# Kernel tuning notes

Measured on AMD Instinct MI355X. Metric: run time of the kernel, lower is better.

Reference implementation:

```python
import jax, jax.numpy as jnp
import numpy as np

B, S, D, H = 2, 2048, 1024, 16
HD = D // H
NEG = -9e15


def setup_inputs() -> dict:
    key = jax.random.key(0)
    ks = jax.random.split(key, 4)
    x = jax.random.normal(ks[0], (B, S, D), dtype=jnp.float32)
    # causal mask, broadcastable over batch and heads
    mask = jnp.tril(jnp.ones((S, S), dtype=jnp.int32))[None, None]
    W_qkv = jax.random.normal(ks[1], (D, 3 * D), dtype=jnp.float32) * (1.0 / np.sqrt(D))
    b_qkv = jnp.zeros((3 * D,), dtype=jnp.float32)
    W_out = jax.random.normal(ks[2], (D, D), dtype=jnp.float32) * (1.0 / np.sqrt(D))
    b_out = jnp.zeros((D,), dtype=jnp.float32)
    return {"x": x, "mask": mask, "W_qkv": W_qkv, "b_qkv": b_qkv,
            "W_out": W_out, "b_out": b_out}


def reference(x, mask, W_qkv, b_qkv, W_out, b_out):
    b, s, _ = x.shape
    qkv = x @ W_qkv + b_qkv                       # [B,S,3D]
    qkv = qkv.reshape(b, s, H, 3 * HD)            # per-head interleaved qkv
    qkv = jnp.transpose(qkv, (0, 2, 1, 3))        # [B,H,S,3*HD]
    q, k, v = jnp.split(qkv, 3, axis=-1)          # each [B,H,S,HD]
    scores = jnp.einsum('bhqd,bhkd->bhqk', q, k) / np.sqrt(HD)
    scores = jnp.where(mask == 0, jnp.float32(NEG), scores)
    attn = jax.nn.softmax(scores, axis=-1)
    out = jnp.einsum('bhqk,bhkd->bhqd', attn, v)  # [B,H,S,HD]
    out = jnp.transpose(out, (0, 2, 1, 3)).reshape(b, s, H * HD)
    return out @ W_out + b_out
```

## Files before the change

### kernel.cpp

```cpp
#include <hip/hip_runtime.h>
#include <math.h>

constexpr int Bb = 2, Ss = 2048, Dd = 1024, Hh = 16, HDd = 64;

typedef __attribute__((ext_vector_type(8))) short bf16x8;
typedef __attribute__((ext_vector_type(4))) float f32x4;
typedef __attribute__((ext_vector_type(8))) unsigned short u16x8;
typedef __attribute__((ext_vector_type(4))) unsigned short u16x4;

__device__ __forceinline__ unsigned short bf16_rn(float f) {
  unsigned int u = __float_as_uint(f);
  u += 0x7fffu + ((u >> 16) & 1u);
  return (unsigned short)(u >> 16);
}
__device__ __forceinline__ float bf16_f(unsigned short h) {
  return __uint_as_float(((unsigned int)h) << 16);
}

__global__ __launch_bounds__(256) void split_f32(
    const float* __restrict__ in, unsigned short* __restrict__ hi,
    unsigned short* __restrict__ lo, int n8) {
  int i = blockIdx.x * 256 + threadIdx.x;
  if (i >= n8) return;
  const float4* p = (const float4*)in + (size_t)i * 2;
  float4 a = p[0], b = p[1];
  float v[8] = {a.x, a.y, a.z, a.w, b.x, b.y, b.z, b.w};
  u16x8 h, l;
  #pragma unroll
  for (int j = 0; j < 8; j++) {
    unsigned short hb = bf16_rn(v[j]);
    h[j] = hb;
    l[j] = bf16_rn(v[j] - bf16_f(hb));
  }
  *(u16x8*)(hi + (size_t)i * 8) = h;
  *(u16x8*)(lo + (size_t)i * 8) = l;
}

__global__ __launch_bounds__(256) void transpose_split_f32(
    const float* __restrict__ W, unsigned short* __restrict__ Thi,
    unsigned short* __restrict__ Tlo, int K, int N) {
  __shared__ float tile[32][33];
  int n0 = blockIdx.x * 32, k0 = blockIdx.y * 32;
  int t = threadIdx.x;
  #pragma unroll
  for (int p = 0; p < 4; p++) {
    int idx = t + p * 256;
    int kk = idx >> 5, nn = idx & 31;
    tile[kk][nn] = W[(size_t)(k0 + kk) * N + n0 + nn];
  }
  __syncthreads();
  #pragma unroll
  for (int p = 0; p < 4; p++) {
    int idx = t + p * 256;
    int nn = idx >> 5, kk = idx & 31;
    float v = tile[kk][nn];
    unsigned short hb = bf16_rn(v);
    size_t o = (size_t)(n0 + nn) * K + k0 + kk;
    Thi[o] = hb;
    Tlo[o] = bf16_rn(v - bf16_f(hb));
  }
}

typedef __attribute__((address_space(3))) unsigned int lds_u32;
typedef const __attribute__((address_space(1))) unsigned int glb_u32;
__device__ __forceinline__ void gload16(const void* g, void* l) {
  __builtin_amdgcn_global_load_lds((glb_u32*)g, (lds_u32*)l, 16, 0, 0);
}

#define GEMM_CORE(KD)                                                          \
  __shared__ unsigned short lds[4 * 4096];                                     \
  const int tid = threadIdx.x;                                                 \
  const int lane = tid & 63, wid = tid >> 6;                                   \
  const int m0 = blockIdx.y * 128, n0 = blockIdx.x * 128;                      \
  const int wrow = wid >> 1, wcol = wid & 1;                                   \
  const int lrow = lane & 15, g = lane >> 4;                                   \
  const int o0 = wid * 128 + lane, o1 = o0 + 64;                               \
  const int r0 = o0 >> 2, G0 = (o0 & 3) ^ ((r0 >> 1) & 3);                     \
  const int r1 = o1 >> 2, G1 = (o1 & 3) ^ ((r1 >> 1) & 3);                     \
  const unsigned short* sA0h = Ahi + (size_t)(m0 + r0) * KD + G0 * 8;          \
  const unsigned short* sA1h = Ahi + (size_t)(m0 + r1) * KD + G1 * 8;          \
  const unsigned short* sA0l = Alo + (size_t)(m0 + r0) * KD + G0 * 8;          \
  const unsigned short* sA1l = Alo + (size_t)(m0 + r1) * KD + G1 * 8;          \
  const unsigned short* sB0h = Bhi + (size_t)(n0 + r0) * KD + G0 * 8;          \
  const unsigned short* sB1h = Bhi + (size_t)(n0 + r1) * KD + G1 * 8;          \
  const unsigned short* sB0l = Blo + (size_t)(n0 + r0) * KD + G0 * 8;          \
  const unsigned short* sB1l = Blo + (size_t)(n0 + r1) * KD + G1 * 8;          \
  unsigned short* dA0h = lds + 0 + wid * 1024;                                 \
  unsigned short* dA1h = dA0h + 512;                                           \
  unsigned short* dA0l = lds + 4096 + wid * 1024;                              \
  unsigned short* dA1l = dA0l + 512;                                           \
  unsigned short* dB0h = lds + 8192 + wid * 1024;                              \
  unsigned short* dB1h = dB0h + 512;                                           \
  unsigned short* dB0l = lds + 12288 + wid * 1024;                             \
  unsigned short* dB1l = dB0l + 512;                                           \
  int offA[4], offB[4];                                                        \
  _Pragma("unroll")                                                            \
  for (int m = 0; m < 4; m++) {                                                \
    int row = wrow * 64 + m * 16 + lrow;                                       \
    offA[m] = row * 32 + ((g ^ ((row >> 1) & 3)) * 8);                         \
  }                                                                            \
  _Pragma("unroll")                                                            \
  for (int n = 0; n < 4; n++) {                                                \
    int row = wcol * 64 + n * 16 + lrow;                                       \
    offB[n] = row * 32 + ((g ^ ((row >> 1) & 3)) * 8);                         \
  }                                                                            \
  f32x4 acc[4][4];                                                             \
  _Pragma("unroll")                                                            \
  for (int m = 0; m < 4; m++)                                                  \
    _Pragma("unroll")                                                          \
    for (int n = 0; n < 4; n++) acc[m][n] = (f32x4){0.f, 0.f, 0.f, 0.f};       \
  for (int k0 = 0; k0 < KD; k0 += 32) {                                        \
    gload16(sA0h + k0, dA0h); gload16(sA1h + k0, dA1h);                        \
    gload16(sA0l + k0, dA0l); gload16(sA1l + k0, dA1l);                        \
    gload16(sB0h + k0, dB0h); gload16(sB1h + k0, dB1h);                        \
    gload16(sB0l + k0, dB0l); gload16(sB1l + k0, dB1l);                        \
    __syncthreads();                                                           \
    bf16x8 ah[4], al[4], bh[4], bl[4];                                         \
    _Pragma("unroll")                                                          \
    for (int m = 0; m < 4; m++) {                                              \
      ah[m] = *(const bf16x8*)(lds + 0 + offA[m]);                             \
      al[m] = *(const bf16x8*)(lds + 4096 + offA[m]);                          \
    }                                                                          \
    _Pragma("unroll")                                                          \
    for (int n = 0; n < 4; n++) {                                              \
      bh[n] = *(const bf16x8*)(lds + 8192 + offB[n]);                          \
      bl[n] = *(const bf16x8*)(lds + 12288 + offB[n]);                         \
    }                                                                          \
    _Pragma("unroll")                                                          \
    for (int m = 0; m < 4; m++)                                                \
      _Pragma("unroll")                                                        \
      for (int n = 0; n < 4; n++) {                                            \
        acc[m][n] = __builtin_amdgcn_mfma_f32_16x16x32_bf16(ah[m], bh[n], acc[m][n], 0, 0, 0); \
        acc[m][n] = __builtin_amdgcn_mfma_f32_16x16x32_bf16(ah[m], bl[n], acc[m][n], 0, 0, 0); \
        acc[m][n] = __builtin_amdgcn_mfma_f32_16x16x32_bf16(al[m], bh[n], acc[m][n], 0, 0, 0); \
      }                                                                        \
    __syncthreads();                                                           \
  }

template<int KD>
__global__ __launch_bounds__(256) void gemm_split_bf16(
    const unsigned short* __restrict__ Ahi, const unsigned short* __restrict__ Alo,
    const unsigned short* __restrict__ Bhi, const unsigned short* __restrict__ Blo,
    const float* __restrict__ bias, float* __restrict__ C, int N)
{
  GEMM_CORE(KD)
  #pragma unroll
  for (int n = 0; n < 4; n++) {
    int gcol = n0 + wcol * 64 + n * 16 + lrow;
    float bv = bias[gcol];
    #pragma unroll
    for (int m = 0; m < 4; m++) {
      f32x4 a = acc[m][n];
      #pragma unroll
      for (int r = 0; r < 4; r++) {
        int grow = m0 + wrow * 64 + m * 16 + g * 4 + r;
        C[(size_t)grow * N + gcol] = a[r] + bv;
      }
    }
  }
}

template<int KD>
__global__ __launch_bounds__(256) void gemm_qkv(
    const unsigned short* __restrict__ Ahi, const unsigned short* __restrict__ Alo,
    const unsigned short* __restrict__ Bhi, const unsigned short* __restrict__ Blo,
    const float* __restrict__ bias,
    unsigned short* __restrict__ Qh, unsigned short* __restrict__ Ql,
    unsigned short* __restrict__ Kh, unsigned short* __restrict__ Kl,
    unsigned short* __restrict__ Vth, unsigned short* __restrict__ Vtl)
{
  GEMM_CORE(KD)
  const int bidx = m0 >> 11;
  const int sbase = (m0 & 2047) + wrow * 64 + g * 4;
  #pragma unroll
  for (int n = 0; n < 4; n++) {
    int gcol = n0 + wcol * 64 + n * 16 + lrow;
    unsigned hh = (unsigned)gcol / 192u;
    int inner = gcol - (int)hh * 192;
    int part = inner >> 6;
    int d = inner & 63;
    float bv = bias[gcol];
    size_t base = (size_t)(bidx * 16 + (int)hh) * 131072;
    #pragma unroll
    for (int m = 0; m < 4; m++) {
      f32x4 a = acc[m][n];
      int s0 = sbase + m * 16;
      if (part == 0) {
        #pragma unroll
        for (int r = 0; r < 4; r++) {
          float v = (a[r] + bv) * 0.18033688011112042f;
          unsigned short hi = bf16_rn(v);
          size_t ix = base + (size_t)(s0 + r) * 64 + d;
          Qh[ix] = hi; Ql[ix] = bf16_rn(v - bf16_f(hi));
        }
      } else if (part == 1) {
        #pragma unroll
        for (int r = 0; r < 4; r++) {
          float v = a[r] + bv;
          unsigned short hi = bf16_rn(v);
          size_t ix = base + (size_t)(s0 + r) * 64 + d;
          Kh[ix] = hi; Kl[ix] = bf16_rn(v - bf16_f(hi));
        }
      } else {
        u16x4 hv, lv;
        #pragma unroll
        for (int r = 0; r < 4; r++) {
          float v = a[r] + bv;
          hv[r] = bf16_rn(v);
          lv[r] = bf16_rn(v - bf16_f(hv[r]));
        }
        size_t ix = base + (size_t)d * 2048 + s0;
        *(u16x4*)(Vth + ix) = hv;
        *(u16x4*)(Vtl + ix) = lv;
      }
    }
  }
}

__global__ __launch_bounds__(512) void flash_attn_mfma(
    const unsigned short* __restrict__ Qh, const unsigned short* __restrict__ Ql,
    const unsigned short* __restrict__ Kh, const unsigned short* __restrict__ Kl,
    const unsigned short* __restrict__ Vth, const unsigned short* __restrict__ Vtl,
    unsigned short* __restrict__ atthi, unsigned short* __restrict__ attlo)
{
  const int pidx = blockIdx.x;
  const int h = blockIdx.y, b = blockIdx.z;
  const int bh = b * Hh + h;
  const int NT = Ss / 128;
  const int qtA = pidx, qtB = NT - 1 - pidx;
  const int tid = threadIdx.x, lane = tid & 63, wid = tid >> 6;
  const int q0w = (wid < 4) ? (qtA * 128 + wid * 32)
                            : (qtB * 128 + (wid - 4) * 32);
  const int lrow = lane & 15, lg = lane >> 4;

  __shared__ unsigned short KH[2][4096], KL[2][4096], VH[2][4096], VL[2][4096];
  __shared__ unsigned short Pbuf[8][2048];

  const size_t hb = (size_t)bh * 131072;
  const unsigned short* qhb = Qh + hb;
  const unsigned short* qlb = Ql + hb;
  const unsigned short* khb = Kh + hb;
  const unsigned short* klb = Kl + hb;
  const unsigned short* vhb = Vth + hb;
  const unsigned short* vlb = Vtl + hb;

  bf16x8 qfh[2][2], qfl[2][2];
  #pragma unroll
  for (int mi = 0; mi < 2; mi++)
    #pragma unroll
    for (int ks = 0; ks < 2; ks++) {
      int off = (q0w + mi * 16 + lrow) * 64 + ks * 32 + lg * 8;
      qfh[mi][ks] = *(const bf16x8*)(qhb + off);
      qfl[mi][ks] = *(const bf16x8*)(qlb + off);
    }

  int offK[4][2], offP[2][2];
  #pragma unroll
  for (int ci = 0; ci < 4; ci++)
    #pragma unroll
    for (int ks = 0; ks < 2; ks++) {
      int row = ci * 16 + lrow;
      offK[ci][ks] = row * 64 + (((ks * 4 + lg) ^ (row & 7)) * 8);
    }
  #pragma unroll
  for (int mi = 0; mi < 2; mi++)
    #pragma unroll
    for (int ks = 0; ks < 2; ks++) {
      int row = mi * 16 + lrow;
      offP[mi][ks] = row * 64 + (((ks * 4 + lg) ^ (row & 7)) * 8);
    }

  const int sr = tid >> 3, sg = ((tid & 7) ^ ((tid >> 3) & 7)) * 8;

  float m_[2][4], l_[2][4];
  f32x4 oacc[2][4];
  #pragma unroll
  for (int mi = 0; mi < 2; mi++)
    #pragma unroll
    for (int r = 0; r < 4; r++) { m_[mi][r] = -INFINITY; l_[mi][r] = 0.f; }
  #pragma unroll
  for (int mi = 0; mi < 2; mi++)
    #pragma unroll
    for (int di = 0; di < 4; di++) oacc[mi][di] = (f32x4){0.f, 0.f, 0.f, 0.f};

  unsigned short* Pw = Pbuf[wid];
  const int nt = 2 * (qtB + 1);

  gload16(khb + (size_t)sr * 64 + sg, KH[0] + wid * 512);
  gload16(klb + (size_t)sr * 64 + sg, KL[0] + wid * 512);
  gload16(vhb + (size_t)sr * 2048 + sg, VH[0] + wid * 512);
  gload16(vlb + (size_t)sr * 2048 + sg, VL[0] + wid * 512);
  __syncthreads();

  for (int t = 0; t < nt; ++t) {
    const int kv0 = t * 64;
    if (t + 1 < nt) {
      const int nb = (t + 1) & 1;
      const int nk = kv0 + 64;
      gload16(khb + (size_t)(nk + sr) * 64 + sg, KH[nb] + wid * 512);
      gload16(klb + (size_t)(nk + sr) * 64 + sg, KL[nb] + wid * 512);
      gload16(vhb + (size_t)sr * 2048 + nk + sg, VH[nb] + wid * 512);
      gload16(vlb + (size_t)sr * 2048 + nk + sg, VL[nb] + wid * 512);
    }

    if (kv0 <= q0w + 31) {
      const int cb = t & 1;
      const unsigned short* KHc = KH[cb];
      const unsigned short* KLc = KL[cb];
      const unsigned short* VHc = VH[cb];
      const unsigned short* VLc = VL[cb];

      f32x4 sf[2][4];
      #pragma unroll
      for (int mi = 0; mi < 2; mi++)
        #pragma unroll
        for (int ci = 0; ci < 4; ci++) sf[mi][ci] = (f32x4){0.f, 0.f, 0.f, 0.f};
      __builtin_amdgcn_s_setprio(1);
      #pragma unroll
      for (int ci = 0; ci < 4; ci++) {
        bf16x8 kh0 = *(const bf16x8*)(KHc + offK[ci][0]);
        bf16x8 kh1 = *(const bf16x8*)(KHc + offK[ci][1]);
        bf16x8 kl0 = *(const bf16x8*)(KLc + offK[ci][0]);
        bf16x8 kl1 = *(const bf16x8*)(KLc + offK[ci][1]);
        #pragma unroll
        for (int mi = 0; mi < 2; mi++) {
          f32x4 s = sf[mi][ci];
          s = __builtin_amdgcn_mfma_f32_16x16x32_bf16(qfh[mi][0], kh0, s, 0, 0, 0);
          s = __builtin_amdgcn_mfma_f32_16x16x32_bf16(qfh[mi][1], kh1, s, 0, 0, 0);
          s = __builtin_amdgcn_mfma_f32_16x16x32_bf16(qfh[mi][0], kl0, s, 0, 0, 0);
          s = __builtin_amdgcn_mfma_f32_16x16x32_bf16(qfh[mi][1], kl1, s, 0, 0, 0);
          s = __builtin_amdgcn_mfma_f32_16x16x32_bf16(qfl[mi][0], kh0, s, 0, 0, 0);
          s = __builtin_amdgcn_mfma_f32_16x16x32_bf16(qfl[mi][1], kh1, s, 0, 0, 0);
          sf[mi][ci] = s;
        }
      }
      __builtin_amdgcn_s_setprio(0);

      if (kv0 + 63 > q0w) {
        #pragma unroll
        for (int mi = 0; mi < 2; mi++)
          #pragma unroll
          for (int ci = 0; ci < 4; ci++)
            #pragma unroll
            for (int r = 0; r < 4; r++) {
              int q = q0w + mi * 16 + lg * 4 + r;
              int kv = kv0 + ci * 16 + lrow;
              if (kv > q) sf[mi][ci][r] = -1e30f;
            }
      }

      #pragma unroll
      for (int mi = 0; mi < 2; mi++)
        #pragma unroll
        for (int r = 0; r < 4; r++) {
          float mx = fmaxf(fmaxf(sf[mi][0][r], sf[mi][1][r]),
                           fmaxf(sf[mi][2][r], sf[mi][3][r]));
          mx = fmaxf(mx, __shfl_xor(mx, 1));
          mx = fmaxf(mx, __shfl_xor(mx, 2));
          mx = fmaxf(mx, __shfl_xor(mx, 4));
          mx = fmaxf(mx, __shfl_xor(mx, 8));
          float mn = fmaxf(m_[mi][r], mx);
          float alpha = __builtin_amdgcn_exp2f(m_[mi][r] - mn);
          m_[mi][r] = mn;
          float rs = 0.f;
          #pragma unroll
          for (int ci = 0; ci < 4; ci++) {
            float p = __builtin_amdgcn_exp2f(sf[mi][ci][r] - mn);
            sf[mi][ci][r] = p;
            rs += p;
          }
          rs += __shfl_xor(rs, 1);
          rs += __shfl_xor(rs, 2);
          rs += __shfl_xor(rs, 4);
          rs += __shfl_xor(rs, 8);
          l_[mi][r] = l_[mi][r] * alpha + rs;
          #pragma unroll
          for (int di = 0; di < 4; di++) oacc[mi][di][r] *= alpha;
        }

      #pragma unroll
      for (int mi = 0; mi < 2; mi++)
        #pragma unroll
        for (int ci = 0; ci < 4; ci++) {
          int colb = ci * 16 + lrow;
          int gcol = colb >> 3, crem = colb & 7;
          #pragma unroll
          for (int r = 0; r < 4; r++) {
            int rr = mi * 16 + lg * 4 + r;
            Pw[rr * 64 + ((gcol ^ (rr & 7)) * 8) + crem] = bf16_rn(sf[mi][ci][r]);
          }
        }

      bf16x8 pa[2][2];
      #pragma unroll
      for (int mi = 0; mi < 2; mi++)
        #pragma unroll
        for (int ks = 0; ks < 2; ks++)
          pa[mi][ks] = *(const bf16x8*)(Pw + offP[mi][ks]);
      __builtin_amdgcn_s_setprio(1);
      #pragma unroll
      for (int di = 0; di < 4; di++) {
        bf16x8 vh0 = *(const bf16x8*)(VHc + offK[di][0]);
        bf16x8 vh1 = *(const bf16x8*)(VHc + offK[di][1]);
        bf16x8 vl0 = *(const bf16x8*)(VLc + offK[di][0]);
        bf16x8 vl1 = *(const bf16x8*)(VLc + offK[di][1]);
        #pragma unroll
        for (int mi = 0; mi < 2; mi++) {
          f32x4 o = oacc[mi][di];
          o = __builtin_amdgcn_mfma_f32_16x16x32_bf16(pa[mi][0], vh0, o, 0, 0, 0);
          o = __builtin_amdgcn_mfma_f32_16x16x32_bf16(pa[mi][1], vh1, o, 0, 0, 0);
          o = __builtin_amdgcn_mfma_f32_16x16x32_bf16(pa[mi][0], vl0, o, 0, 0, 0);
          o = __builtin_amdgcn_mfma_f32_16x16x32_bf16(pa[mi][1], vl1, o, 0, 0, 0);
          oacc[mi][di] = o;
        }
      }
      __builtin_amdgcn_s_setprio(0);
    }
    __syncthreads();
  }

  #pragma unroll
  for (int mi = 0; mi < 2; mi++) {
    float inv[4];
    #pragma unroll
    for (int r = 0; r < 4; r++) inv[r] = 1.f / l_[mi][r];
    #pragma unroll
    for (int di = 0; di < 4; di++) {
      f32x4 o = oacc[mi][di];
      #pragma unroll
      for (int r = 0; r < 4; r++) {
        float v = o[r] * inv[r];
        int srow = q0w + mi * 16 + lg * 4 + r;
        size_t idx = ((size_t)b * Ss + srow) * 1024 + h * 64 + di * 16 + lrow;
        unsigned short hi = bf16_rn(v);
        atthi[idx] = hi;
        attlo[idx] = bf16_rn(v - bf16_f(hi));
      }
    }
  }
}

extern "C" void kernel_launch(void* const* d_in, const int* in_sizes, int n_in,
                              void* d_out, int out_size, void* d_ws, size_t ws_size,
                              hipStream_t stream) {
  const float* x    = (const float*)d_in[0];
  const float* Wqkv = (const float*)d_in[2];
  const float* bqkv = (const float*)d_in[3];
  const float* Wout = (const float*)d_in[4];
  const float* bout = (const float*)d_in[5];
  float* out = (float*)d_out;

  char* ws = (char*)d_ws;
  unsigned short* Qh  = (unsigned short*)(ws);
  unsigned short* Ql  = (unsigned short*)(ws + 8388608);
  unsigned short* Kh  = (unsigned short*)(ws + 16777216);
  unsigned short* Kl  = (unsigned short*)(ws + 25165824);
  unsigned short* Vth = (unsigned short*)(ws + 33554432);
  unsigned short* Vtl = (unsigned short*)(ws + 41943040);
  unsigned short* atthi = (unsigned short*)(ws + 50331648);
  unsigned short* attlo = (unsigned short*)(ws + 58720256);
  unsigned short* xhi = (unsigned short*)(ws + 67108864);
  unsigned short* xlo = (unsigned short*)(ws + 75497472);
  unsigned short* wqh = (unsigned short*)(ws + 83886080);
  unsigned short* wql = (unsigned short*)(ws + 90177536);
  unsigned short* woh = (unsigned short*)(ws + 96468992);
  unsigned short* wol = (unsigned short*)(ws + 98566144);

  const int M = Bb * Ss;

  split_f32<<<(M * Dd / 8) / 256, 256, 0, stream>>>(x, xhi, xlo, M * Dd / 8);
  transpose_split_f32<<<dim3(3 * Dd / 32, Dd / 32), 256, 0, stream>>>(Wqkv, wqh, wql, Dd, 3 * Dd);
  transpose_split_f32<<<dim3(Dd / 32, Dd / 32), 256, 0, stream>>>(Wout, woh, wol, Dd, Dd);

  gemm_qkv<1024><<<dim3(3 * Dd / 128, M / 128), 256, 0, stream>>>(
      xhi, xlo, wqh, wql, bqkv, Qh, Ql, Kh, Kl, Vth, Vtl);

  flash_attn_mfma<<<dim3(Ss / 256, Hh, Bb), 512, 0, stream>>>(
      Qh, Ql, Kh, Kl, Vth, Vtl, atthi, attlo);

  gemm_split_bf16<1024><<<dim3(Dd / 128, M / 128), 256, 0, stream>>>(
      atthi, attlo, woh, wol, bout, out, Dd);
}
```

Before: 355.5 us.

## Double-buffer split-bf16 GEMMs with 512-thread blocks and larger QKV tiles

Replaces the single-buffered GEMM macro with a templated core that prefetches the next K-slice into a second LDS buffer using global_load_lds, with explicit vmcnt waits and raw barriers. It uses 8 waves per block, a 256x192 tile for the QKV projection and a 128x128 tile with 8 waves for the output projection, and raises MFMA wave priority with s_setprio. The aim is to overlap global loads with MFMA work and to raise data reuse per block. In exchange it uses more LDS and registers (24 accumulators per wave in QKV), and the QKV grid shrinks to 256 blocks, which may leave the CU array partly idle.

```diff
diff --git a/kernel.cpp b/kernel.cpp
--- a/kernel.cpp
+++ b/kernel.cpp
@@ -67,101 +67,154 @@
   __builtin_amdgcn_global_load_lds((glb_u32*)g, (lds_u32*)l, 16, 0, 0);
 }
 
-#define GEMM_CORE(KD)                                                          \
-  __shared__ unsigned short lds[4 * 4096];                                     \
-  const int tid = threadIdx.x;                                                 \
-  const int lane = tid & 63, wid = tid >> 6;                                   \
-  const int m0 = blockIdx.y * 128, n0 = blockIdx.x * 128;                      \
-  const int wrow = wid >> 1, wcol = wid & 1;                                   \
-  const int lrow = lane & 15, g = lane >> 4;                                   \
-  const int o0 = wid * 128 + lane, o1 = o0 + 64;                               \
-  const int r0 = o0 >> 2, G0 = (o0 & 3) ^ ((r0 >> 1) & 3);                     \
-  const int r1 = o1 >> 2, G1 = (o1 & 3) ^ ((r1 >> 1) & 3);                     \
-  const unsigned short* sA0h = Ahi + (size_t)(m0 + r0) * KD + G0 * 8;          \
-  const unsigned short* sA1h = Ahi + (size_t)(m0 + r1) * KD + G1 * 8;          \
-  const unsigned short* sA0l = Alo + (size_t)(m0 + r0) * KD + G0 * 8;          \
-  const unsigned short* sA1l = Alo + (size_t)(m0 + r1) * KD + G1 * 8;          \
-  const unsigned short* sB0h = Bhi + (size_t)(n0 + r0) * KD + G0 * 8;          \
-  const unsigned short* sB1h = Bhi + (size_t)(n0 + r1) * KD + G1 * 8;          \
-  const unsigned short* sB0l = Blo + (size_t)(n0 + r0) * KD + G0 * 8;          \
-  const unsigned short* sB1l = Blo + (size_t)(n0 + r1) * KD + G1 * 8;          \
-  unsigned short* dA0h = lds + 0 + wid * 1024;                                 \
-  unsigned short* dA1h = dA0h + 512;                                           \
-  unsigned short* dA0l = lds + 4096 + wid * 1024;                              \
-  unsigned short* dA1l = dA0l + 512;                                           \
-  unsigned short* dB0h = lds + 8192 + wid * 1024;                              \
-  unsigned short* dB1h = dB0h + 512;                                           \
-  unsigned short* dB0l = lds + 12288 + wid * 1024;                             \
-  unsigned short* dB1l = dB0l + 512;                                           \
-  int offA[4], offB[4];                                                        \
-  _Pragma("unroll")                                                            \
-  for (int m = 0; m < 4; m++) {                                                \
-    int row = wrow * 64 + m * 16 + lrow;                                       \
-    offA[m] = row * 32 + ((g ^ ((row >> 1) & 3)) * 8);                         \
-  }                                                                            \
-  _Pragma("unroll")                                                            \
-  for (int n = 0; n < 4; n++) {                                                \
-    int row = wcol * 64 + n * 16 + lrow;                                       \
-    offB[n] = row * 32 + ((g ^ ((row >> 1) & 3)) * 8);                         \
-  }                                                                            \
-  f32x4 acc[4][4];                                                             \
-  _Pragma("unroll")                                                            \
-  for (int m = 0; m < 4; m++)                                                  \
-    _Pragma("unroll")                                                          \
-    for (int n = 0; n < 4; n++) acc[m][n] = (f32x4){0.f, 0.f, 0.f, 0.f};       \
-  for (int k0 = 0; k0 < KD; k0 += 32) {                                        \
-    gload16(sA0h + k0, dA0h); gload16(sA1h + k0, dA1h);                        \
-    gload16(sA0l + k0, dA0l); gload16(sA1l + k0, dA1l);                        \
-    gload16(sB0h + k0, dB0h); gload16(sB1h + k0, dB1h);                        \
-    gload16(sB0l + k0, dB0l); gload16(sB1l + k0, dB1l);                        \
-    __syncthreads();                                                           \
-    bf16x8 ah[4], al[4], bh[4], bl[4];                                         \
-    _Pragma("unroll")                                                          \
-    for (int m = 0; m < 4; m++) {                                              \
-      ah[m] = *(const bf16x8*)(lds + 0 + offA[m]);                             \
-      al[m] = *(const bf16x8*)(lds + 4096 + offA[m]);                          \
-    }                                                                          \
-    _Pragma("unroll")                                                          \
-    for (int n = 0; n < 4; n++) {                                              \
-      bh[n] = *(const bf16x8*)(lds + 8192 + offB[n]);                          \
-      bl[n] = *(const bf16x8*)(lds + 12288 + offB[n]);                         \
-    }                                                                          \
-    _Pragma("unroll")                                                          \
-    for (int m = 0; m < 4; m++)                                                \
-      _Pragma("unroll")                                                        \
-      for (int n = 0; n < 4; n++) {                                            \
-        acc[m][n] = __builtin_amdgcn_mfma_f32_16x16x32_bf16(ah[m], bh[n], acc[m][n], 0, 0, 0); \
-        acc[m][n] = __builtin_amdgcn_mfma_f32_16x16x32_bf16(ah[m], bl[n], acc[m][n], 0, 0, 0); \
-        acc[m][n] = __builtin_amdgcn_mfma_f32_16x16x32_bf16(al[m], bh[n], acc[m][n], 0, 0, 0); \
-      }                                                                        \
-    __syncthreads();                                                           \
-  }
-
-template<int KD>
-__global__ __launch_bounds__(256) void gemm_split_bf16(
+__device__ __forceinline__ void syncb() {
+  asm volatile("" ::: "memory");
+  __builtin_amdgcn_s_barrier();
+  asm volatile("" ::: "memory");
+}
+template<int N> __device__ __forceinline__ void wait_vmcnt() {
+  if constexpr (N == 0)      asm volatile("s_waitcnt vmcnt(0)" ::: "memory");
+  else if constexpr (N == 4) asm volatile("s_waitcnt vmcnt(4)" ::: "memory");
+  else if constexpr (N == 7) asm volatile("s_waitcnt vmcnt(7)" ::: "memory");
+}
+
+template<int BM, int BN>
+__device__ __forceinline__ void gemm_core256(
     const unsigned short* __restrict__ Ahi, const unsigned short* __restrict__ Alo,
     const unsigned short* __restrict__ Bhi, const unsigned short* __restrict__ Blo,
-    const float* __restrict__ bias, float* __restrict__ C, int N)
+    int KD, f32x4 (&acc)[BM / 32][BN / 64])
 {
-  GEMM_CORE(KD)
-  #pragma unroll
-  for (int n = 0; n < 4; n++) {
-    int gcol = n0 + wcol * 64 + n * 16 + lrow;
-    float bv = bias[gcol];
-    #pragma unroll
-    for (int m = 0; m < 4; m++) {
-      f32x4 a = acc[m][n];
-      #pragma unroll
-      for (int r = 0; r < 4; r++) {
-        int grow = m0 + wrow * 64 + m * 16 + g * 4 + r;
-        C[(size_t)grow * N + gcol] = a[r] + bv;
-      }
-    }
-  }
-}
-
-template<int KD>
-__global__ __launch_bounds__(256) void gemm_qkv(
+  constexpr int MF = BM / 32, NF = BN / 64;
+  constexpr int NA = BM / 64, NB = BN / 64;
+  constexpr int NV = NA + NB;
+  constexpr int AELT = 2 * BM * 32;
+  constexpr int BELT = 2 * BN * 32;
+  constexpr int ALO = BM * 32, BLO = BN * 32;
+  __shared__ unsigned short lds[2][AELT + BELT];
+
+  const int tid = threadIdx.x, lane = tid & 63, wid = tid >> 6;
+  const int m0 = blockIdx.y * BM, n0 = blockIdx.x * BN;
+  const int wrow = wid >> 2, wcol = wid & 3;
+  const int lrow = lane & 15, g = lane >> 4;
+
+  const unsigned short* srcA[NA]; int dstA[NA];
+  #pragma unroll
+  for (int i = 0; i < NA; i++) {
+    int gi = tid + i * 512;
+    int lr = gi >> 2, s = gi & 3, gs = s ^ ((lr >> 1) & 3);
+    const unsigned short* bp = (lr < BM) ? Ahi : Alo;
+    int row = (lr < BM) ? lr : lr - BM;
+    srcA[i] = bp + (size_t)(m0 + row) * KD + gs * 8;
+    dstA[i] = (gi & ~63) * 8;
+  }
+  const unsigned short* srcB[NB]; int dstB[NB];
+  #pragma unroll
+  for (int i = 0; i < NB; i++) {
+    int gi = tid + i * 512;
+    int lr = gi >> 2, s = gi & 3, gs = s ^ ((lr >> 1) & 3);
+    const unsigned short* bp = (lr < BN) ? Bhi : Blo;
+    int row = (lr < BN) ? lr : lr - BN;
+    srcB[i] = bp + (size_t)(n0 + row) * KD + gs * 8;
+    dstB[i] = AELT + (gi & ~63) * 8;
+  }
+
+  int offA[MF], offB[NF];
+  #pragma unroll
+  for (int m = 0; m < MF; m++) {
+    int row = wrow * (BM / 2) + m * 16 + lrow;
+    offA[m] = row * 32 + ((g ^ ((row >> 1) & 3)) * 8);
+  }
+  #pragma unroll
+  for (int n = 0; n < NF; n++) {
+    int row = wcol * (BN / 4) + n * 16 + lrow;
+    offB[n] = AELT + row * 32 + ((g ^ ((row >> 1) & 3)) * 8);
+  }
+
+  #pragma unroll
+  for (int m = 0; m < MF; m++)
+    #pragma unroll
+    for (int n = 0; n < NF; n++) acc[m][n] = (f32x4){0.f, 0.f, 0.f, 0.f};
+
+  const int nk = KD / 32;
+
+  #pragma unroll
+  for (int i = 0; i < NA; i++) gload16(srcA[i], &lds[0][dstA[i]]);
+  #pragma unroll
+  for (int i = 0; i < NB; i++) gload16(srcB[i], &lds[0][dstB[i]]);
+  #pragma unroll
+  for (int i = 0; i < NA; i++) gload16(srcA[i] + 32, &lds[1][dstA[i]]);
+  #pragma unroll
+  for (int i = 0; i < NB; i++) gload16(srcB[i] + 32, &lds[1][dstB[i]]);
+  wait_vmcnt<NV>();
+  syncb();
+
+  for (int t = 0; t < nk; ++t) {
+    const unsigned short* L = lds[t & 1];
+
+    bf16x8 bh[NF], bl[NF];
+    #pragma unroll
+    for (int n = 0; n < NF; n++) {
+      bh[n] = *(const bf16x8*)(L + offB[n]);
+      bl[n] = *(const bf16x8*)(L + offB[n] + BLO);
+    }
+    {
+      bf16x8 ah[MF / 2], al[MF / 2];
+      #pragma unroll
+      for (int m = 0; m < MF / 2; m++) {
+        ah[m] = *(const bf16x8*)(L + offA[m]);
+        al[m] = *(const bf16x8*)(L + offA[m] + ALO);
+      }
+      __builtin_amdgcn_s_setprio(1);
+      #pragma unroll
+      for (int m = 0; m < MF / 2; m++)
+        #pragma unroll
+        for (int n = 0; n < NF; n++) {
+          acc[m][n] = __builtin_amdgcn_mfma_f32_16x16x32_bf16(ah[m], bh[n], acc[m][n], 0, 0, 0);
+          acc[m][n] = __builtin_amdgcn_mfma_f32_16x16x32_bf16(ah[m], bl[n], acc[m][n], 0, 0, 0);
+          acc[m][n] = __builtin_amdgcn_mfma_f32_16x16x32_bf16(al[m], bh[n], acc[m][n], 0, 0, 0);
+        }
+      __builtin_amdgcn_s_setprio(0);
+    }
+    syncb();
+    {
+      bf16x8 ah[MF / 2], al[MF / 2];
+      #pragma unroll
+      for (int m = 0; m < MF / 2; m++) {
+        ah[m] = *(const bf16x8*)(L + offA[m + MF / 2]);
+        al[m] = *(const bf16x8*)(L + offA[m + MF / 2] + ALO);
+      }
+      __builtin_amdgcn_s_setprio(1);
+      #pragma unroll
+      for (int m = 0; m < MF / 2; m++)
+        #pragma unroll
+        for (int n = 0; n < NF; n++) {
+          acc[m + MF / 2][n] = __builtin_amdgcn_mfma_f32_16x16x32_bf16(ah[m], bh[n], acc[m + MF / 2][n], 0, 0, 0);
+          acc[m + MF / 2][n] = __builtin_amdgcn_mfma_f32_16x16x32_bf16(ah[m], bl[n], acc[m + MF / 2][n], 0, 0, 0);
+          acc[m + MF / 2][n] = __builtin_amdgcn_mfma_f32_16x16x32_bf16(al[m], bh[n], acc[m + MF / 2][n], 0, 0, 0);
+        }
+      __builtin_amdgcn_s_setprio(0);
+    }
+
+    if (t + 1 < nk) {
+      asm volatile("s_waitcnt lgkmcnt(0)" ::: "memory");
+      syncb();
+      if (t + 2 < nk) {
+        const int koff = (t + 2) * 32;
+        unsigned short* W = lds[t & 1];
+        #pragma unroll
+        for (int i = 0; i < NA; i++) gload16(srcA[i] + koff, W + dstA[i]);
+        #pragma unroll
+        for (int i = 0; i < NB; i++) gload16(srcB[i] + koff, W + dstB[i]);
+        wait_vmcnt<NV>();
+      } else {
+        wait_vmcnt<0>();
+      }
+      syncb();
+    }
+  }
+}
+
+__global__ __launch_bounds__(512) void gemm_qkv256(
     const unsigned short* __restrict__ Ahi, const unsigned short* __restrict__ Alo,
     const unsigned short* __restrict__ Bhi, const unsigned short* __restrict__ Blo,
     const float* __restrict__ bias,
@@ -169,12 +222,18 @@
     unsigned short* __restrict__ Kh, unsigned short* __restrict__ Kl,
     unsigned short* __restrict__ Vth, unsigned short* __restrict__ Vtl)
 {
-  GEMM_CORE(KD)
+  f32x4 acc[8][3];
+  gemm_core256<256, 192>(Ahi, Alo, Bhi, Blo, 1024, acc);
+
+  const int tid = threadIdx.x, lane = tid & 63, wid = tid >> 6;
+  const int lrow = lane & 15, g = lane >> 4;
+  const int m0 = blockIdx.y * 256, n0 = blockIdx.x * 192;
+  const int wrow = wid >> 2, wcol = wid & 3;
   const int bidx = m0 >> 11;
-  const int sbase = (m0 & 2047) + wrow * 64 + g * 4;
-  #pragma unroll
-  for (int n = 0; n < 4; n++) {
-    int gcol = n0 + wcol * 64 + n * 16 + lrow;
+  const int sbase = (m0 & 2047) + wrow * 128 + g * 4;
+  #pragma unroll
+  for (int n = 0; n < 3; n++) {
+    int gcol = n0 + wcol * 48 + n * 16 + lrow;
     unsigned hh = (unsigned)gcol / 192u;
     int inner = gcol - (int)hh * 192;
     int part = inner >> 6;
@@ -182,7 +241,7 @@
     float bv = bias[gcol];
     size_t base = (size_t)(bidx * 16 + (int)hh) * 131072;
     #pragma unroll
-    for (int m = 0; m < 4; m++) {
+    for (int m = 0; m < 8; m++) {
       f32x4 a = acc[m][n];
       int s0 = sbase + m * 16;
       if (part == 0) {
@@ -212,6 +271,34 @@
         size_t ix = base + (size_t)d * 2048 + s0;
         *(u16x4*)(Vth + ix) = hv;
         *(u16x4*)(Vtl + ix) = lv;
+      }
+    }
+  }
+}
+
+__global__ __launch_bounds__(512) void gemm_out256(
+    const unsigned short* __restrict__ Ahi, const unsigned short* __restrict__ Alo,
+    const unsigned short* __restrict__ Bhi, const unsigned short* __restrict__ Blo,
+    const float* __restrict__ bias, float* __restrict__ C)
+{
+  f32x4 acc[4][2];
+  gemm_core256<128, 128>(Ahi, Alo, Bhi, Blo, 1024, acc);
+
+  const int tid = threadIdx.x, lane = tid & 63, wid = tid >> 6;
+  const int lrow = lane & 15, g = lane >> 4;
+  const int m0 = blockIdx.y * 128, n0 = blockIdx.x * 128;
+  const int wrow = wid >> 2, wcol = wid & 3;
+  #pragma unroll
+  for (int n = 0; n < 2; n++) {
+    int gcol = n0 + wcol * 32 + n * 16 + lrow;
+    float bv = bias[gcol];
+    #pragma unroll
+    for (int m = 0; m < 4; m++) {
+      f32x4 a = acc[m][n];
+      #pragma unroll
+      for (int r = 0; r < 4; r++) {
+        int grow = m0 + wrow * 64 + m * 16 + g * 4 + r;
+        C[(size_t)grow * 1024 + gcol] = a[r] + bv;
       }
     }
   }
@@ -472,12 +559,12 @@
   transpose_split_f32<<<dim3(3 * Dd / 32, Dd / 32), 256, 0, stream>>>(Wqkv, wqh, wql, Dd, 3 * Dd);
   transpose_split_f32<<<dim3(Dd / 32, Dd / 32), 256, 0, stream>>>(Wout, woh, wol, Dd, Dd);
 
-  gemm_qkv<1024><<<dim3(3 * Dd / 128, M / 128), 256, 0, stream>>>(
+  gemm_qkv256<<<dim3(16, 16), 512, 0, stream>>>(
       xhi, xlo, wqh, wql, bqkv, Qh, Ql, Kh, Kl, Vth, Vtl);
 
   flash_attn_mfma<<<dim3(Ss / 256, Hh, Bb), 512, 0, stream>>>(
       Qh, Ql, Kh, Kl, Vth, Vtl, atthi, attlo);
 
-  gemm_split_bf16<1024><<<dim3(Dd / 128, M / 128), 256, 0, stream>>>(
-      atthi, attlo, woh, wol, bout, out, Dd);
-}
+  gemm_out256<<<dim3(8, 32), 512, 0, stream>>>(
+      atthi, attlo, woh, wol, bout, out);
+}
```

Measured after the change: 312.3 us. 12.2% less time.
